# Kernel optimization log

Measured on AMD Instinct MI355X. Metric: run time of the kernel, lower is better.

## Reference

```python
import jax, jax.numpy as jnp
import numpy as np
from jax import lax

K = 7       # kernel_size (window)
G = 8       # groups
C = 64      # out_channels


def _unfold(y):
    # y: (B, C, H+2p, W+2p) already padded by p = K//2
    # returns windows: (B, C, H, W, K, K)  == torch unfold(2,K,1).unfold(3,K,1)
    p = lax.conv_general_dilated_patches(y, (K, K), (1, 1), 'VALID')
    B, _, H, W = p.shape
    # patch channel order: (C, kh, kw)
    return p.reshape(B, C, K, K, H, W).transpose(0, 1, 4, 5, 2, 3)


def setup_inputs() -> dict:
    key = jax.random.key(0)
    ks = jax.random.split(key, 6)
    return {
        'x': jax.random.normal(ks[0], (4, 64, 56, 56), jnp.float32),
        'Wq': jax.random.normal(ks[1], (64, 64), jnp.float32) * 0.05,
        'Wk': jax.random.normal(ks[2], (64, 64), jnp.float32) * 0.05,
        'Wv': jax.random.normal(ks[3], (64, 64), jnp.float32) * 0.05,
        'rel_h': jax.random.normal(ks[4], (32, 1, 1, 7, 1), jnp.float32),
        'rel_w': jax.random.normal(ks[5], (32, 1, 1, 1, 7), jnp.float32),
    }


def reference(x, Wq, Wk, Wv, rel_h, rel_w):
    B, Cin, H, W = x.shape
    pad = K // 2
    # 1x1 convs (bias=False)
    q = jnp.einsum('oi,bihw->bohw', Wq, x)               # (B,C,H,W)
    k = jnp.einsum('oi,bihw->bohw', Wk, x)
    v = jnp.einsum('oi,bihw->bohw', Wv, x)
    # pad spatially by K//2, extract KxK windows per pixel
    spad = ((0, 0), (0, 0), (pad, pad), (pad, pad))
    k_w = _unfold(jnp.pad(k, spad))                       # (B,C,H,W,K,K)
    v_w = _unfold(jnp.pad(v, spad))                       # (B,C,H,W,K,K)
    # add relative positional embeddings to value halves
    v_h, v_w2 = jnp.split(v_w, 2, axis=1)
    v_w = jnp.concatenate((v_h + rel_h[None], v_w2 + rel_w[None]), axis=1)
    # group reshape: (B,G,C/G,H,W,K*K)
    k_w = k_w.reshape(B, G, C // G, H, W, K * K)
    v_w = v_w.reshape(B, G, C // G, H, W, K * K)
    q = q.reshape(B, G, C // G, H, W, 1)
    # per-channel elementwise scores, softmax over window, weighted sum
    attn = jax.nn.softmax(q * k_w, axis=-1)
    out = jnp.einsum('bgchwk,bgchwk->bgchw', attn, v_w)
    return out.reshape(B, C, H, W)
```

## Files before the change

kernel.cpp:

```cpp
#include <hip/hip_runtime.h>
#include <stdint.h>

#define HW    56
#define CH    64
#define PIX   (HW*HW)
#define KS    7
#define PAD   3
#define TS    8
#define HALO  14
#define HP    (HALO*HALO)
#define NPT   13
#define XLD   68
#define KVLD  67

#define OFF_QS  26264
#define OFF_W   30616
#define OFF_REL 36760
#define LDS_F   37208

typedef __attribute__((ext_vector_type(8))) short short8;
typedef __attribute__((ext_vector_type(4))) float f32x4;

__device__ __forceinline__ uint32_t rne_bf16(float v) {
    uint32_t u = __float_as_uint(v);
    return (u + 0x7FFFu + ((u >> 16) & 1u)) >> 16;
}
__device__ __forceinline__ float fexp2(float x) {
    float r;
    asm("v_exp_f32 %0, %1" : "=v"(r) : "v"(x));
    return r;
}

__global__ __launch_bounds__(1024) void fused_attn(
    const float* __restrict__ x,  const float* __restrict__ Wq,
    const float* __restrict__ Wk, const float* __restrict__ Wv,
    const float* __restrict__ rel_h, const float* __restrict__ rel_w,
    float* __restrict__ out)
{
    __shared__ __align__(16) float lds[LDS_F];
    float2* kv   = (float2*)lds;
    float*  xs   = lds;
    float*  qs   = lds + OFF_QS;
    short8* wlds = (short8*)(lds + OFF_W);
    float*  rlds = lds + OFF_REL;

    const int t    = threadIdx.x;
    const int b    = blockIdx.x / 49;
    const int tile = blockIdx.x % 49;
    const int ty0  = (tile / 7) * TS;
    const int tx0  = (tile % 7) * TS;

    {
        const int hx = t & 15;
        const int ci = t >> 4;
        const int gx = tx0 + hx - PAD;
        const bool okx = (hx < HALO) & (gx >= 0) & (gx < HW);
        const float* xb = x + (size_t)(b * CH + ci) * PIX;
        #pragma unroll
        for (int it = 0; it < HALO; ++it) {
            int gy = ty0 + it - PAD;
            bool ok = okx & (gy >= 0) & (gy < HW);
            float v = ok ? xb[gy * HW + gx] : 0.f;
            if (hx < HALO)
                xs[(it * HALO + hx) * XLD + ci] = v;
        }
    }
    if (t < 768)
        xs[(HP + (t >> 6)) * XLD + (t & 63)] = 0.f;
    #pragma unroll
    for (int k = 0; k < 2; ++k) {
        int u = t + k * 1024;
        if (u < 1536) {
            int m = u >> 9, cot = (u >> 7) & 3, ch = (u >> 6) & 1, l2 = u & 63;
            const float* Wm = (m == 0) ? Wk : (m == 1) ? Wv : Wq;
            const float* src = &Wm[(cot * 16 + (l2 & 15)) * 64 + ch * 32 + (l2 >> 4) * 8];
            float4 f0 = *(const float4*)src;
            float4 f1 = *(const float4*)(src + 4);
            short8 h;
            h[0] = (short)rne_bf16(f0.x); h[1] = (short)rne_bf16(f0.y);
            h[2] = (short)rne_bf16(f0.z); h[3] = (short)rne_bf16(f0.w);
            h[4] = (short)rne_bf16(f1.x); h[5] = (short)rne_bf16(f1.y);
            h[6] = (short)rne_bf16(f1.z); h[7] = (short)rne_bf16(f1.w);
            wlds[u] = h;
        }
    }
    if (t < 448)
        rlds[t] = (t < 224) ? rel_h[t] : rel_w[t - 224];
    __syncthreads();

    const int l  = t & 63;
    const int w  = t >> 6;
    const int lr = l & 15;
    const int lk = l >> 4;

    short8 aH[2], aL[2];
    if (w < NPT) {
        int arow = w * 16 + lr;
        #pragma unroll
        for (int ch = 0; ch < 2; ++ch) {
            const float* src = &xs[arow * XLD + ch * 32 + lk * 8];
            float4 f0 = *(const float4*)src;
            float4 f1 = *(const float4*)(src + 4);
            float vv[8] = {f0.x, f0.y, f0.z, f0.w, f1.x, f1.y, f1.z, f1.w};
            short8 h, lo;
            #pragma unroll
            for (int j = 0; j < 8; ++j) {
                uint32_t hb = rne_bf16(vv[j]);
                h[j]  = (short)hb;
                lo[j] = (short)rne_bf16(vv[j] - __uint_as_float(hb << 16));
            }
            aH[ch] = h; aL[ch] = lo;
        }
    }
    __syncthreads();

    #pragma unroll
    for (int m = 0; m < 3; ++m) {
        if (w < NPT) {
            short8 bh[4][2];
            #pragma unroll
            for (int cot = 0; cot < 4; ++cot)
                #pragma unroll
                for (int ch = 0; ch < 2; ++ch)
                    bh[cot][ch] = wlds[((m * 4 + cot) * 2 + ch) * 64 + l];
            #pragma unroll
            for (int cot = 0; cot < 4; ++cot) {
                f32x4 a = {0.f, 0.f, 0.f, 0.f};
                a = __builtin_amdgcn_mfma_f32_16x16x32_bf16(aL[0], bh[cot][0], a, 0, 0, 0);
                a = __builtin_amdgcn_mfma_f32_16x16x32_bf16(aH[0], bh[cot][0], a, 0, 0, 0);
                a = __builtin_amdgcn_mfma_f32_16x16x32_bf16(aL[1], bh[cot][1], a, 0, 0, 0);
                a = __builtin_amdgcn_mfma_f32_16x16x32_bf16(aH[1], bh[cot][1], a, 0, 0, 0);
                const int co = cot * 16 + lr;
                #pragma unroll
                for (int r = 0; r < 4; ++r) {
                    int px = w * 16 + lk * 4 + r;
                    if (px < HP) {
                        if (m == 0)      kv[px * KVLD + co].x = a[r];
                        else if (m == 1) kv[px * KVLD + co].y = a[r];
                        else {
                            int py = px / HALO, pxx = px % HALO;
                            if (py >= PAD && py < PAD + TS &&
                                pxx >= PAD && pxx < PAD + TS)
                                qs[((py - PAD) * TS + (pxx - PAD)) * XLD + co] = a[r];
                        }
                    }
                }
            }
        }
    }
    __syncthreads();

    const int c    = ((w & 1) << 5) | (l & 31);
    const int quad = ((w >> 1) << 1) | (l >> 5);
    const int oy   = quad & 7;
    const int half = quad >> 3;
    const bool is_h = ((w & 1) == 0);

    float relv[KS];
    #pragma unroll
    for (int j = 0; j < KS; ++j)
        relv[j] = rlds[(is_h ? 0 : 224) + (c & 31) * KS + j];

    float qv[4], sum[4], acc[4], racc[4];
    #pragma unroll
    for (int ox = 0; ox < 4; ++ox) {
        qv[ox] = qs[(oy * TS + half * 4 + ox) * XLD + c] * 1.44269504088896f;
        sum[ox] = 0.f; acc[ox] = 0.f; racc[ox] = 0.f;
    }

    #pragma unroll
    for (int kh = 0; kh < KS; ++kh) {
        const int prow0 = (oy + kh) * HALO + half * 4;
        float2 row[10];
        #pragma unroll
        for (int ii = 0; ii < 10; ++ii)
            row[ii] = kv[(prow0 + ii) * KVLD + c];
        const float rh = relv[kh];
        if (is_h) {
            #pragma unroll
            for (int ox = 0; ox < 4; ++ox) {
                float esum = 0.f;
                #pragma unroll
                for (int kw = 0; kw < KS; ++kw) {
                    float2 f = row[ox + kw];
                    float e = fexp2(qv[ox] * f.x);
                    esum += e;
                    acc[ox] = fmaf(e, f.y, acc[ox]);
                }
                sum[ox] += esum;
                racc[ox] = fmaf(rh, esum, racc[ox]);
            }
        } else {
            #pragma unroll
            for (int ox = 0; ox < 4; ++ox) {
                #pragma unroll
                for (int kw = 0; kw < KS; ++kw) {
                    float2 f = row[ox + kw];
                    float e = fexp2(qv[ox] * f.x);
                    sum[ox] += e;
                    acc[ox]  = fmaf(e, f.y, acc[ox]);
                    racc[ox] = fmaf(e, relv[kw], racc[ox]);
                }
            }
        }
    }
    __syncthreads();

    float* os = qs;
    #pragma unroll
    for (int ox = 0; ox < 4; ++ox)
        os[(oy * TS + half * 4 + ox) * XLD + c] =
            (acc[ox] + racc[ox]) * __builtin_amdgcn_rcpf(sum[ox]);
    __syncthreads();
    #pragma unroll
    for (int k2 = 0; k2 < 4; ++k2) {
        int idx = t + 1024 * k2;
        int p   = idx & 63;
        int cc  = idx >> 6;
        out[(b * CH + cc) * PIX + (ty0 + (p >> 3)) * HW + tx0 + (p & 7)] =
            os[p * XLD + cc];
    }
}

extern "C" void kernel_launch(void* const* d_in, const int* in_sizes, int n_in,
                              void* d_out, int out_size, void* d_ws, size_t ws_size,
                              hipStream_t stream) {
    const float* x     = (const float*)d_in[0];
    const float* Wq    = (const float*)d_in[1];
    const float* Wk    = (const float*)d_in[2];
    const float* Wv    = (const float*)d_in[3];
    const float* rel_h = (const float*)d_in[4];
    const float* rel_w = (const float*)d_in[5];
    float* out = (float*)d_out;

    fused_attn<<<196, 1024, 0, stream>>>(x, Wq, Wk, Wv, rel_h, rel_w, out);
}
```

Baseline: 23.39 us.

## Split each tile's channels across four blocks to fill more compute units

```diff
diff --git a/kernel.cpp b/kernel.cpp
--- a/kernel.cpp
+++ b/kernel.cpp
@@ -8,15 +8,17 @@
 #define PAD   3
 #define TS    8
 #define HALO  14
-#define HP    (HALO*HALO)
+#define HP    196
 #define NPT   13
 #define XLD   68
-#define KVLD  67
-
-#define OFF_QS  26264
-#define OFF_W   30616
-#define OFF_REL 36760
-#define LDS_F   37208
+#define NCH   16
+#define KVLD  17
+#define QLD   17
+
+#define F_Q    6664
+#define F_W    14144
+#define F_REL  15680
+#define F_TOT  15792
 
 typedef __attribute__((ext_vector_type(8))) short short8;
 typedef __attribute__((ext_vector_type(4))) float f32x4;
@@ -31,61 +33,72 @@
     return r;
 }
 
-__global__ __launch_bounds__(1024) void fused_attn(
+__global__ __launch_bounds__(512, 4) void fused_attn(
     const float* __restrict__ x,  const float* __restrict__ Wq,
     const float* __restrict__ Wk, const float* __restrict__ Wv,
     const float* __restrict__ rel_h, const float* __restrict__ rel_w,
     float* __restrict__ out)
 {
-    __shared__ __align__(16) float lds[LDS_F];
-    float2* kv   = (float2*)lds;
-    float*  xs   = lds;
-    float*  qs   = lds + OFF_QS;
-    short8* wlds = (short8*)(lds + OFF_W);
-    float*  rlds = lds + OFF_REL;
-
-    const int t    = threadIdx.x;
-    const int b    = blockIdx.x / 49;
-    const int tile = blockIdx.x % 49;
+    __shared__ __align__(16) float lds[F_TOT];
+    float2* kv = (float2*)lds;
+    float*  xs = lds;
+    float*  ql = lds + F_Q;
+    short8* wl = (short8*)(lds + F_W);
+    float*  rl = lds + F_REL;
+
+    const int orig = blockIdx.x;
+    const int swz  = (orig & 7) * 98 + (orig >> 3);
+    const int b    = swz / 196;
+    const int rem  = swz % 196;
+    const int tile = rem >> 2;
+    const int quad = rem & 3;
     const int ty0  = (tile / 7) * TS;
     const int tx0  = (tile % 7) * TS;
+    const int c0   = quad * NCH;
+    const bool is_h = (quad < 2);
+
+    const int t = threadIdx.x;
 
     {
         const int hx = t & 15;
-        const int ci = t >> 4;
+        const int u  = t >> 4;
         const int gx = tx0 + hx - PAD;
         const bool okx = (hx < HALO) & (gx >= 0) & (gx < HW);
-        const float* xb = x + (size_t)(b * CH + ci) * PIX;
         #pragma unroll
-        for (int it = 0; it < HALO; ++it) {
-            int gy = ty0 + it - PAD;
-            bool ok = okx & (gy >= 0) & (gy < HW);
-            float v = ok ? xb[gy * HW + gx] : 0.f;
+        for (int it = 0; it < 28; ++it) {
+            int jj = u + 32 * it;
+            int gy = jj >> 6;
+            int ci = jj & 63;
+            int iy = ty0 + gy - PAD;
+            float v = 0.f;
+            if (okx & (iy >= 0) & (iy < HW))
+                v = x[(b * CH + ci) * PIX + iy * HW + gx];
             if (hx < HALO)
-                xs[(it * HALO + hx) * XLD + ci] = v;
-        }
-    }
-    if (t < 768)
-        xs[(HP + (t >> 6)) * XLD + (t & 63)] = 0.f;
+                xs[(gy * HALO + hx) * XLD + ci] = v;
+        }
+    }
     #pragma unroll
     for (int k = 0; k < 2; ++k) {
-        int u = t + k * 1024;
-        if (u < 1536) {
-            int m = u >> 9, cot = (u >> 7) & 3, ch = (u >> 6) & 1, l2 = u & 63;
-            const float* Wm = (m == 0) ? Wk : (m == 1) ? Wv : Wq;
-            const float* src = &Wm[(cot * 16 + (l2 & 15)) * 64 + ch * 32 + (l2 >> 4) * 8];
-            float4 f0 = *(const float4*)src;
-            float4 f1 = *(const float4*)(src + 4);
-            short8 h;
-            h[0] = (short)rne_bf16(f0.x); h[1] = (short)rne_bf16(f0.y);
-            h[2] = (short)rne_bf16(f0.z); h[3] = (short)rne_bf16(f0.w);
-            h[4] = (short)rne_bf16(f1.x); h[5] = (short)rne_bf16(f1.y);
-            h[6] = (short)rne_bf16(f1.z); h[7] = (short)rne_bf16(f1.w);
-            wlds[u] = h;
-        }
-    }
-    if (t < 448)
-        rlds[t] = (t < 224) ? rel_h[t] : rel_w[t - 224];
+        int u = t + 512 * k;
+        if (u < 768)
+            xs[(HP + (u >> 6)) * XLD + (u & 63)] = 0.f;
+    }
+    if (t < 384) {
+        int m = t >> 7, ch = (t >> 6) & 1, l2 = t & 63;
+        const float* Wm = (m == 0) ? Wk : (m == 1) ? Wv : Wq;
+        const float* src = &Wm[(c0 + (l2 & 15)) * 64 + ch * 32 + (l2 >> 4) * 8];
+        float4 f0 = *(const float4*)src;
+        float4 f1 = *(const float4*)(src + 4);
+        short8 h;
+        h[0] = (short)rne_bf16(f0.x); h[1] = (short)rne_bf16(f0.y);
+        h[2] = (short)rne_bf16(f0.z); h[3] = (short)rne_bf16(f0.w);
+        h[4] = (short)rne_bf16(f1.x); h[5] = (short)rne_bf16(f1.y);
+        h[6] = (short)rne_bf16(f1.z); h[7] = (short)rne_bf16(f1.w);
+        wl[(m * 2 + ch) * 64 + l2] = h;
+    }
+    if (t < 112)
+        rl[t] = is_h ? rel_h[(quad & 1) * 112 + t]
+                     : rel_w[(quad - 2) * 112 + t];
     __syncthreads();
 
     const int l  = t & 63;
@@ -93,55 +106,56 @@
     const int lr = l & 15;
     const int lk = l >> 4;
 
-    short8 aH[2], aL[2];
-    if (w < NPT) {
-        int arow = w * 16 + lr;
+    short8 aH[2][2], aL[2][2];
+    #pragma unroll
+    for (int i = 0; i < 2; ++i) {
+        int pt = w + 8 * i;
+        if (pt < NPT) {
+            int arow = pt * 16 + lr;
+            #pragma unroll
+            for (int ch = 0; ch < 2; ++ch) {
+                const float* src = &xs[arow * XLD + ch * 32 + lk * 8];
+                float4 f0 = *(const float4*)src;
+                float4 f1 = *(const float4*)(src + 4);
+                float vv[8] = {f0.x, f0.y, f0.z, f0.w, f1.x, f1.y, f1.z, f1.w};
+                short8 h, lo;
+                #pragma unroll
+                for (int j = 0; j < 8; ++j) {
+                    uint32_t hb = rne_bf16(vv[j]);
+                    h[j]  = (short)hb;
+                    lo[j] = (short)rne_bf16(vv[j] - __uint_as_float(hb << 16));
+                }
+                aH[i][ch] = h; aL[i][ch] = lo;
+            }
+        }
+    }
+    __syncthreads();
+
+    #pragma unroll
+    for (int m = 0; m < 3; ++m) {
+        short8 bh0 = wl[(m * 2 + 0) * 64 + l];
+        short8 bh1 = wl[(m * 2 + 1) * 64 + l];
         #pragma unroll
-        for (int ch = 0; ch < 2; ++ch) {
-            const float* src = &xs[arow * XLD + ch * 32 + lk * 8];
-            float4 f0 = *(const float4*)src;
-            float4 f1 = *(const float4*)(src + 4);
-            float vv[8] = {f0.x, f0.y, f0.z, f0.w, f1.x, f1.y, f1.z, f1.w};
-            short8 h, lo;
-            #pragma unroll
-            for (int j = 0; j < 8; ++j) {
-                uint32_t hb = rne_bf16(vv[j]);
-                h[j]  = (short)hb;
-                lo[j] = (short)rne_bf16(vv[j] - __uint_as_float(hb << 16));
-            }
-            aH[ch] = h; aL[ch] = lo;
-        }
-    }
-    __syncthreads();
-
-    #pragma unroll
-    for (int m = 0; m < 3; ++m) {
-        if (w < NPT) {
-            short8 bh[4][2];
-            #pragma unroll
-            for (int cot = 0; cot < 4; ++cot)
-                #pragma unroll
-                for (int ch = 0; ch < 2; ++ch)
-                    bh[cot][ch] = wlds[((m * 4 + cot) * 2 + ch) * 64 + l];
-            #pragma unroll
-            for (int cot = 0; cot < 4; ++cot) {
+        for (int i = 0; i < 2; ++i) {
+            int pt = w + 8 * i;
+            if (pt < NPT) {
                 f32x4 a = {0.f, 0.f, 0.f, 0.f};
-                a = __builtin_amdgcn_mfma_f32_16x16x32_bf16(aL[0], bh[cot][0], a, 0, 0, 0);
-                a = __builtin_amdgcn_mfma_f32_16x16x32_bf16(aH[0], bh[cot][0], a, 0, 0, 0);
-                a = __builtin_amdgcn_mfma_f32_16x16x32_bf16(aL[1], bh[cot][1], a, 0, 0, 0);
-                a = __builtin_amdgcn_mfma_f32_16x16x32_bf16(aH[1], bh[cot][1], a, 0, 0, 0);
-                const int co = cot * 16 + lr;
+                a = __builtin_amdgcn_mfma_f32_16x16x32_bf16(aL[i][0], bh0, a, 0, 0, 0);
+                a = __builtin_amdgcn_mfma_f32_16x16x32_bf16(aH[i][0], bh0, a, 0, 0, 0);
+                a = __builtin_amdgcn_mfma_f32_16x16x32_bf16(aL[i][1], bh1, a, 0, 0, 0);
+                a = __builtin_amdgcn_mfma_f32_16x16x32_bf16(aH[i][1], bh1, a, 0, 0, 0);
                 #pragma unroll
                 for (int r = 0; r < 4; ++r) {
-                    int px = w * 16 + lk * 4 + r;
+                    int px = pt * 16 + lk * 4 + r;
                     if (px < HP) {
-                        if (m == 0)      kv[px * KVLD + co].x = a[r];
-                        else if (m == 1) kv[px * KVLD + co].y = a[r];
+                        if (m == 0)      kv[px * KVLD + lr].x = a[r];
+                        else if (m == 1) kv[px * KVLD + lr].y = a[r];
                         else {
                             int py = px / HALO, pxx = px % HALO;
                             if (py >= PAD && py < PAD + TS &&
                                 pxx >= PAD && pxx < PAD + TS)
-                                qs[((py - PAD) * TS + (pxx - PAD)) * XLD + co] = a[r];
+                                ql[((py - PAD) * TS + (pxx - PAD)) * QLD + lr] =
+                                    a[r] * 1.44269504088896f;
                         }
                     }
                 }
@@ -150,75 +164,68 @@
     }
     __syncthreads();
 
-    const int c    = ((w & 1) << 5) | (l & 31);
-    const int quad = ((w >> 1) << 1) | (l >> 5);
-    const int oy   = quad & 7;
-    const int half = quad >> 3;
-    const bool is_h = ((w & 1) == 0);
+    const int cc4 = t & 15;
+    const int oxb = ((t >> 4) & 3) * 2;
+    const int oyy = t >> 6;
 
     float relv[KS];
     #pragma unroll
     for (int j = 0; j < KS; ++j)
-        relv[j] = rlds[(is_h ? 0 : 224) + (c & 31) * KS + j];
-
-    float qv[4], sum[4], acc[4], racc[4];
-    #pragma unroll
-    for (int ox = 0; ox < 4; ++ox) {
-        qv[ox] = qs[(oy * TS + half * 4 + ox) * XLD + c] * 1.44269504088896f;
-        sum[ox] = 0.f; acc[ox] = 0.f; racc[ox] = 0.f;
-    }
+        relv[j] = rl[cc4 * KS + j];
+
+    float qv[2], sum[2] = {0.f, 0.f}, acc[2] = {0.f, 0.f}, racc[2] = {0.f, 0.f};
+    qv[0] = ql[(oyy * TS + oxb) * QLD + cc4];
+    qv[1] = ql[(oyy * TS + oxb + 1) * QLD + cc4];
 
     #pragma unroll
     for (int kh = 0; kh < KS; ++kh) {
-        const int prow0 = (oy + kh) * HALO + half * 4;
-        float2 row[10];
+        const int rb = (oyy + kh) * HALO + oxb;
+        float2 row[8];
         #pragma unroll
-        for (int ii = 0; ii < 10; ++ii)
-            row[ii] = kv[(prow0 + ii) * KVLD + c];
+        for (int ii = 0; ii < 8; ++ii)
+            row[ii] = kv[(rb + ii) * KVLD + cc4];
         const float rh = relv[kh];
         if (is_h) {
             #pragma unroll
-            for (int ox = 0; ox < 4; ++ox) {
-                float esum = 0.f;
+            for (int e = 0; e < 2; ++e) {
+                float es = 0.f;
                 #pragma unroll
                 for (int kw = 0; kw < KS; ++kw) {
-                    float2 f = row[ox + kw];
-                    float e = fexp2(qv[ox] * f.x);
-                    esum += e;
-                    acc[ox] = fmaf(e, f.y, acc[ox]);
-                }
-                sum[ox] += esum;
-                racc[ox] = fmaf(rh, esum, racc[ox]);
+                    float ee = fexp2(qv[e] * row[e + kw].x);
+                    es += ee;
+                    acc[e] = fmaf(ee, row[e + kw].y, acc[e]);
+                }
+                sum[e] += es;
+                racc[e] = fmaf(rh, es, racc[e]);
             }
         } else {
             #pragma unroll
-            for (int ox = 0; ox < 4; ++ox) {
+            for (int e = 0; e < 2; ++e) {
                 #pragma unroll
                 for (int kw = 0; kw < KS; ++kw) {
-                    float2 f = row[ox + kw];
-                    float e = fexp2(qv[ox] * f.x);
-                    sum[ox] += e;
-                    acc[ox]  = fmaf(e, f.y, acc[ox]);
-                    racc[ox] = fmaf(e, relv[kw], racc[ox]);
-                }
-            }
-        }
-    }
-    __syncthreads();
-
-    float* os = qs;
-    #pragma unroll
-    for (int ox = 0; ox < 4; ++ox)
-        os[(oy * TS + half * 4 + ox) * XLD + c] =
-            (acc[ox] + racc[ox]) * __builtin_amdgcn_rcpf(sum[ox]);
-    __syncthreads();
-    #pragma unroll
-    for (int k2 = 0; k2 < 4; ++k2) {
-        int idx = t + 1024 * k2;
+                    float ee = fexp2(qv[e] * row[e + kw].x);
+                    sum[e] += ee;
+                    acc[e]  = fmaf(ee, row[e + kw].y, acc[e]);
+                    racc[e] = fmaf(ee, relv[kw], racc[e]);
+                }
+            }
+        }
+    }
+    __syncthreads();
+
+    float* os = ql;
+    os[(oyy * TS + oxb)     * QLD + cc4] =
+        (acc[0] + racc[0]) * __builtin_amdgcn_rcpf(sum[0]);
+    os[(oyy * TS + oxb + 1) * QLD + cc4] =
+        (acc[1] + racc[1]) * __builtin_amdgcn_rcpf(sum[1]);
+    __syncthreads();
+    #pragma unroll
+    for (int k = 0; k < 2; ++k) {
+        int idx = t + 512 * k;
         int p   = idx & 63;
         int cc  = idx >> 6;
-        out[(b * CH + cc) * PIX + (ty0 + (p >> 3)) * HW + tx0 + (p & 7)] =
-            os[p * XLD + cc];
+        out[(b * CH + c0 + cc) * PIX + (ty0 + (p >> 3)) * HW + tx0 + (p & 7)] =
+            os[p * QLD + cc];
     }
 }
 
@@ -233,5 +240,5 @@
     const float* rel_w = (const float*)d_in[5];
     float* out = (float*)d_out;
 
-    fused_attn<<<196, 1024, 0, stream>>>(x, Wq, Wk, Wv, rel_h, rel_w, out);
-}
+    fused_attn<<<784, 512, 0, stream>>>(x, Wq, Wk, Wv, rel_h, rel_w, out);
+}
```

After: 29.53 us. 1.26x slower.
